# Kernel optimization log

Hardware: AMD Instinct MI355X
Metric: run time of the kernel (lower is better)

## Reference

```python
import jax, jax.numpy as jnp
import numpy as np

N_NODES = 50000
N_EDGES = 600000
LATENT = 128
IN_FEAT = 7
STEPS = 3
MLP_LAYERS = 2


def setup_inputs() -> dict:
    key = jax.random.key(0)
    ks = jax.random.split(key, 8)
    s = 0.05
    nodes = jax.random.normal(ks[0], (N_NODES, IN_FEAT), jnp.float32)
    senders = jax.random.randint(ks[1], (N_EDGES,), 0, N_NODES, jnp.int32)
    receivers = jax.random.randint(ks[2], (N_EDGES,), 0, N_NODES, jnp.int32)
    W_embed = jax.random.normal(ks[3], (IN_FEAT, LATENT), jnp.float32) * s
    b_embed = jnp.zeros((LATENT,), jnp.float32)
    mlp_W = jax.random.normal(ks[4], (STEPS, MLP_LAYERS, LATENT, LATENT), jnp.float32) * s
    mlp_b = jnp.zeros((STEPS, MLP_LAYERS, LATENT), jnp.float32)
    ln_scale = jnp.ones((STEPS, LATENT), jnp.float32)
    ln_bias = jnp.zeros((STEPS, LATENT), jnp.float32)
    W_dec = jax.random.normal(ks[5], (LATENT, IN_FEAT), jnp.float32) * s
    b_dec = jnp.zeros((IN_FEAT,), jnp.float32)
    return dict(nodes=nodes, senders=senders, receivers=receivers,
                W_embed=W_embed, b_embed=b_embed, mlp_W=mlp_W, mlp_b=mlp_b,
                ln_scale=ln_scale, ln_bias=ln_bias, W_dec=W_dec, b_dec=b_dec)


def _layer_norm(x, scale, bias, eps=1e-6):
    mu = jnp.mean(x, axis=-1, keepdims=True)
    var = jnp.var(x, axis=-1, keepdims=True)
    return (x - mu) * jax.lax.rsqrt(var + eps) * scale + bias


def reference(nodes, senders, receivers, W_embed, b_embed, mlp_W, mlp_b,
              ln_scale, ln_bias, W_dec, b_dec):
    n = nodes.shape[0]
    # symmetric normalization factors (jraph GraphConvolution default)
    ones = jnp.ones((senders.shape[0],), dtype=nodes.dtype)
    sender_deg = jax.ops.segment_sum(ones, senders, num_segments=n)
    receiver_deg = jax.ops.segment_sum(ones, receivers, num_segments=n)
    inv_sqrt_s = jax.lax.rsqrt(jnp.maximum(sender_deg, 1.0))[:, None]
    inv_sqrt_r = jax.lax.rsqrt(jnp.maximum(receiver_deg, 1.0))[:, None]

    # node embedder
    h = nodes @ W_embed + b_embed  # [N, LATENT]
    for step in range(mlp_W.shape[0]):
        # per-node MLP update (update_node_fn applied before aggregation)
        x = h
        for l in range(mlp_W.shape[1]):
            x = jax.nn.relu(x @ mlp_W[step, l] + mlp_b[step, l])
        # normalized gather -> scatter-sum aggregation
        x = x * inv_sqrt_s
        x = jax.ops.segment_sum(x[senders], receivers, num_segments=n)
        x = x * inv_sqrt_r
        # skip connection + layer norm
        h = _layer_norm(h + x, ln_scale[step], ln_bias[step])
    # decoder back to input feature size
    return h @ W_dec + b_dec  # [N, IN_FEAT]
```

## Files before the change

### kernel.cpp

```cpp
#include <hip/hip_runtime.h>

#define NN 50000
#define NE 600000
#define LAT 128
#define IN_F 7
#define CSR_W 64
#define HSTR 136

typedef __attribute__((ext_vector_type(8))) short bfrag;
typedef __attribute__((ext_vector_type(4))) float ffrag;
typedef __attribute__((ext_vector_type(2))) float f32x2;

__device__ inline unsigned short f2bf(float f) {
    unsigned int u = __float_as_uint(f);
    return (unsigned short)((u + 0x7FFFu + ((u >> 16) & 1u)) >> 16);
}
__device__ inline float bf2f(unsigned int b) { return __uint_as_float(b << 16); }


__global__ void k_prep(const float* __restrict__ W, unsigned short* __restrict__ Wp,
                       unsigned int* __restrict__ cnt) {
    int t = blockIdx.x * 256 + threadIdx.x;
    if (t < NN) cnt[t] = 0;
    if (t < 6 * 8 * 4 * 64) {
        int lane = t & 63;
        int ks = (t >> 6) & 3;
        int nt = (t >> 8) & 7;
        int mat = t >> 11;
        int n = nt * 16 + (lane & 15);
        int k0 = ks * 32 + (lane >> 4) * 8;
        const float* src = W + (size_t)mat * LAT * LAT;
        unsigned long long lo = 0, hi = 0;
#pragma unroll
        for (int j = 0; j < 4; ++j)
            lo |= (unsigned long long)f2bf(src[(k0 + j) * LAT + n]) << (16 * j);
#pragma unroll
        for (int j = 0; j < 4; ++j)
            hi |= (unsigned long long)f2bf(src[(k0 + 4 + j) * LAT + n]) << (16 * j);
        unsigned long long* dst = (unsigned long long*)(Wp + (size_t)t * 8);
        dst[0] = lo; dst[1] = hi;
    }
}


__global__ __launch_bounds__(256) void k_fused1(
    const int* __restrict__ s, const int* __restrict__ r,
    unsigned int* __restrict__ cnt, unsigned short* __restrict__ slot,
    const float* __restrict__ nodes, const float* __restrict__ We,
    const float* __restrict__ be,
    const unsigned short* __restrict__ W0p, const unsigned short* __restrict__ W1p,
    const float* __restrict__ b0, const float* __restrict__ b1,
    unsigned char* __restrict__ x, int build_blocks)
{
    __shared__ unsigned short hs[64][HSTR];
    int tid = threadIdx.x;

    if ((int)blockIdx.x < build_blocks) {
        int i = blockIdx.x * 256 + tid;
        if (i < NE) {
            int ss = s[i], rr = r[i];
            atomicAdd(&cnt[ss], 1u);
            unsigned int p = atomicAdd(&cnt[rr], 0x10000u) >> 16;
            if (p < CSR_W) slot[(size_t)rr * CSR_W + p] = (unsigned short)ss;
        }
        return;
    }

    int brow = ((int)blockIdx.x - build_blocks) * 64;
    int rows = NN - brow; if (rows > 64) rows = 64;

#pragma unroll
    for (int it = 0; it < 8; ++it) {
        int fi = it * 256 + tid;
        int rr = fi >> 5, cc = (fi & 31) << 2;
        if (rr < rows) {
            const float* nr = nodes + (size_t)(brow + rr) * IN_F;
            float o0 = be[cc], o1 = be[cc + 1], o2 = be[cc + 2], o3 = be[cc + 3];
#pragma unroll
            for (int k = 0; k < IN_F; ++k) {
                float nv = nr[k];
                const float* wk = We + k * LAT + cc;
                o0 += nv * wk[0]; o1 += nv * wk[1];
                o2 += nv * wk[2]; o3 += nv * wk[3];
            }
            unsigned long long pk = (unsigned long long)f2bf(o0)
                | ((unsigned long long)f2bf(o1) << 16)
                | ((unsigned long long)f2bf(o2) << 32)
                | ((unsigned long long)f2bf(o3) << 48);
            *(unsigned long long*)&hs[rr][cc] = pk;
        }
    }
    __syncthreads();

    int w = tid >> 6, lane = tid & 63;
    int mrow = w * 16 + (lane & 15);
    int koff = (lane >> 4) * 8;
    int ccol = lane & 15;
    int crow = w * 16 + (lane >> 4) * 4;

    float bia0[8], bia1[8];
#pragma unroll
    for (int nt = 0; nt < 8; ++nt) { bia0[nt] = b0[nt * 16 + ccol]; bia1[nt] = b1[nt * 16 + ccol]; }

    ffrag acc[8];
#pragma unroll
    for (int nt = 0; nt < 8; ++nt) acc[nt] = (ffrag)0.0f;
#pragma unroll
    for (int ks = 0; ks < 4; ++ks) {
        bfrag af = *(const bfrag*)&hs[mrow][ks * 32 + koff];
#pragma unroll
        for (int nt = 0; nt < 8; ++nt) {
            bfrag bf = *(const bfrag*)&W0p[(size_t)(((nt * 4) + ks) * 64 + lane) * 8];
            acc[nt] = __builtin_amdgcn_mfma_f32_16x16x32_bf16(af, bf, acc[nt], 0, 0, 0);
        }
    }
#pragma unroll
    for (int nt = 0; nt < 8; ++nt)
#pragma unroll
        for (int reg = 0; reg < 4; ++reg)
            hs[crow + reg][nt * 16 + ccol] = f2bf(fmaxf(acc[nt][reg] + bia0[nt], 0.f));
    __syncthreads();

#pragma unroll
    for (int nt = 0; nt < 8; ++nt) acc[nt] = (ffrag)0.0f;
#pragma unroll
    for (int ks = 0; ks < 4; ++ks) {
        bfrag af = *(const bfrag*)&hs[mrow][ks * 32 + koff];
#pragma unroll
        for (int nt = 0; nt < 8; ++nt) {
            bfrag bf = *(const bfrag*)&W1p[(size_t)(((nt * 4) + ks) * 64 + lane) * 8];
            acc[nt] = __builtin_amdgcn_mfma_f32_16x16x32_bf16(af, bf, acc[nt], 0, 0, 0);
        }
    }
    __syncthreads();
#pragma unroll
    for (int nt = 0; nt < 8; ++nt)
#pragma unroll
        for (int reg = 0; reg < 4; ++reg)
            hs[crow + reg][nt * 16 + ccol] = f2bf(fmaxf(acc[nt][reg] + bia1[nt], 0.f));
    __syncthreads();

#pragma unroll
    for (int it = 0; it < 8; ++it) {
        int fi = it * 256 + tid;
        int rr = fi >> 5, uc = fi & 31;
        if (rr < rows) {
            unsigned long long pk8 = *(unsigned long long*)&hs[rr][uc * 4];
            float f0 = bf2f((unsigned int)(pk8 & 0xFFFFu));
            float f1 = bf2f((unsigned int)((pk8 >> 16) & 0xFFFFu));
            float f2 = bf2f((unsigned int)((pk8 >> 32) & 0xFFFFu));
            float f3 = bf2f((unsigned int)((pk8 >> 48) & 0xFFFFu));
            int o = __builtin_amdgcn_cvt_pk_fp8_f32(f0, f1, 0, false);
            o = __builtin_amdgcn_cvt_pk_fp8_f32(f2, f3, o, true);
            *(int*)&x[(size_t)(brow + rr) * LAT + uc * 4] = o;
        }
    }
}


__global__ __launch_bounds__(256) void k_mlp2(
    const unsigned short* __restrict__ h,
    const unsigned short* __restrict__ W0p, const unsigned short* __restrict__ W1p,
    const float* __restrict__ b0, const float* __restrict__ b1,
    const unsigned int* __restrict__ cnt,
    unsigned char* __restrict__ x, int M)
{
    __shared__ unsigned short hs[64][HSTR];
    int brow = blockIdx.x * 64;
    int tid = threadIdx.x;
    int rows = M - brow; if (rows > 64) rows = 64;

#pragma unroll
    for (int it = 0; it < 8; ++it) {
        int fi = it * 256 + tid;
        int rr = fi >> 5, cc = (fi & 31) << 2;
        if (rr < rows)
            *(unsigned long long*)&hs[rr][cc] =
                *(const unsigned long long*)&h[(size_t)(brow + rr) * LAT + cc];
    }
    __syncthreads();

    int w = tid >> 6, lane = tid & 63;
    int mrow = w * 16 + (lane & 15);
    int koff = (lane >> 4) * 8;
    int ccol = lane & 15;
    int crow = w * 16 + (lane >> 4) * 4;

    float bia0[8], bia1[8];
#pragma unroll
    for (int nt = 0; nt < 8; ++nt) { bia0[nt] = b0[nt * 16 + ccol]; bia1[nt] = b1[nt * 16 + ccol]; }
    float iv[4];
#pragma unroll
    for (int reg = 0; reg < 4; ++reg) {
        int rw = brow + crow + reg;
        unsigned int ds = cnt[rw < NN ? rw : NN - 1] & 0xFFFFu;
        iv[reg] = rsqrtf((float)(ds > 1 ? ds : 1));
    }

    ffrag acc[8];
#pragma unroll
    for (int nt = 0; nt < 8; ++nt) acc[nt] = (ffrag)0.0f;
#pragma unroll
    for (int ks = 0; ks < 4; ++ks) {
        bfrag af = *(const bfrag*)&hs[mrow][ks * 32 + koff];
#pragma unroll
        for (int nt = 0; nt < 8; ++nt) {
            bfrag bf = *(const bfrag*)&W0p[(size_t)(((nt * 4) + ks) * 64 + lane) * 8];
            acc[nt] = __builtin_amdgcn_mfma_f32_16x16x32_bf16(af, bf, acc[nt], 0, 0, 0);
        }
    }
#pragma unroll
    for (int nt = 0; nt < 8; ++nt)
#pragma unroll
        for (int reg = 0; reg < 4; ++reg)
            hs[crow + reg][nt * 16 + ccol] = f2bf(fmaxf(acc[nt][reg] + bia0[nt], 0.f));
    __syncthreads();

#pragma unroll
    for (int nt = 0; nt < 8; ++nt) acc[nt] = (ffrag)0.0f;
#pragma unroll
    for (int ks = 0; ks < 4; ++ks) {
        bfrag af = *(const bfrag*)&hs[mrow][ks * 32 + koff];
#pragma unroll
        for (int nt = 0; nt < 8; ++nt) {
            bfrag bf = *(const bfrag*)&W1p[(size_t)(((nt * 4) + ks) * 64 + lane) * 8];
            acc[nt] = __builtin_amdgcn_mfma_f32_16x16x32_bf16(af, bf, acc[nt], 0, 0, 0);
        }
    }
    __syncthreads();
#pragma unroll
    for (int nt = 0; nt < 8; ++nt)
#pragma unroll
        for (int reg = 0; reg < 4; ++reg)
            hs[crow + reg][nt * 16 + ccol] =
                f2bf(fmaxf(acc[nt][reg] + bia1[nt], 0.f) * iv[reg]);
    __syncthreads();

#pragma unroll
    for (int it = 0; it < 8; ++it) {
        int fi = it * 256 + tid;
        int rr = fi >> 5, uc = fi & 31;
        if (rr < rows) {
            unsigned long long pk8 = *(unsigned long long*)&hs[rr][uc * 4];
            float f0 = bf2f((unsigned int)(pk8 & 0xFFFFu));
            float f1 = bf2f((unsigned int)((pk8 >> 16) & 0xFFFFu));
            float f2 = bf2f((unsigned int)((pk8 >> 32) & 0xFFFFu));
            float f3 = bf2f((unsigned int)((pk8 >> 48) & 0xFFFFu));
            int o = __builtin_amdgcn_cvt_pk_fp8_f32(f0, f1, 0, false);
            o = __builtin_amdgcn_cvt_pk_fp8_f32(f2, f3, o, true);
            *(int*)&x[(size_t)(brow + rr) * LAT + uc * 4] = o;
        }
    }
}


__global__ __launch_bounds__(256) void k_agg(
    const unsigned char* __restrict__ x, unsigned short* __restrict__ h,
    const float* __restrict__ nodes, const float* __restrict__ We,
    const float* __restrict__ be,
    const unsigned int* __restrict__ cnt, const unsigned short* __restrict__ slot,
    const float* __restrict__ gamma, const float* __restrict__ beta,
    const float* __restrict__ Wd, const float* __restrict__ bd,
    float* __restrict__ outd, int mode)
{
    int lane = threadIdx.x & 63;
    int r = blockIdx.x * 4 + (threadIdx.x >> 6);
    if (r >= NN) return;

    int ct = (int)(cnt[r] >> 16);
    float ir = rsqrtf((float)(ct > 1 ? ct : 1));
    int c = ct > CSR_W ? CSR_W : ct;

    int myidx = (lane < c) ? (int)slot[(size_t)r * CSR_W + lane] : 0;

    int j0 = lane * 2;
    float ax0 = 0.f, ay0 = 0.f, ax1 = 0.f, ay1 = 0.f;
    float ax2 = 0.f, ay2 = 0.f, ax3 = 0.f, ay3 = 0.f;
    float ax4 = 0.f, ay4 = 0.f, ax5 = 0.f, ay5 = 0.f;
    float ax6 = 0.f, ay6 = 0.f, ax7 = 0.f, ay7 = 0.f;
    int e = 0;

    if (mode == 0) {
        float myinv = 0.f;
        if (lane < c) {
            unsigned int ds = cnt[myidx] & 0xFFFFu;
            myinv = rsqrtf((float)(ds > 1 ? ds : 1));
        }
        for (; e + 8 <= c; e += 8) {
            int s0 = __shfl(myidx, e),     s1 = __shfl(myidx, e + 1);
            int s2 = __shfl(myidx, e + 2), s3 = __shfl(myidx, e + 3);
            int s4 = __shfl(myidx, e + 4), s5 = __shfl(myidx, e + 5);
            int s6 = __shfl(myidx, e + 6), s7 = __shfl(myidx, e + 7);
            float w0 = __shfl(myinv, e),     w1 = __shfl(myinv, e + 1);
            float w2 = __shfl(myinv, e + 2), w3 = __shfl(myinv, e + 3);
            float w4 = __shfl(myinv, e + 4), w5 = __shfl(myinv, e + 5);
            float w6 = __shfl(myinv, e + 6), w7 = __shfl(myinv, e + 7);
            unsigned short v0 = *(const unsigned short*)&x[(size_t)s0 * LAT + j0];
            unsigned short v1 = *(const unsigned short*)&x[(size_t)s1 * LAT + j0];
            unsigned short v2 = *(const unsigned short*)&x[(size_t)s2 * LAT + j0];
            unsigned short v3 = *(const unsigned short*)&x[(size_t)s3 * LAT + j0];
            unsigned short v4 = *(const unsigned short*)&x[(size_t)s4 * LAT + j0];
            unsigned short v5 = *(const unsigned short*)&x[(size_t)s5 * LAT + j0];
            unsigned short v6 = *(const unsigned short*)&x[(size_t)s6 * LAT + j0];
            unsigned short v7 = *(const unsigned short*)&x[(size_t)s7 * LAT + j0];
            f32x2 d0 = __builtin_amdgcn_cvt_pk_f32_fp8((int)v0, false);
            f32x2 d1 = __builtin_amdgcn_cvt_pk_f32_fp8((int)v1, false);
            f32x2 d2 = __builtin_amdgcn_cvt_pk_f32_fp8((int)v2, false);
            f32x2 d3 = __builtin_amdgcn_cvt_pk_f32_fp8((int)v3, false);
            f32x2 d4 = __builtin_amdgcn_cvt_pk_f32_fp8((int)v4, false);
            f32x2 d5 = __builtin_amdgcn_cvt_pk_f32_fp8((int)v5, false);
            f32x2 d6 = __builtin_amdgcn_cvt_pk_f32_fp8((int)v6, false);
            f32x2 d7 = __builtin_amdgcn_cvt_pk_f32_fp8((int)v7, false);
            ax0 += d0.x * w0; ay0 += d0.y * w0;
            ax1 += d1.x * w1; ay1 += d1.y * w1;
            ax2 += d2.x * w2; ay2 += d2.y * w2;
            ax3 += d3.x * w3; ay3 += d3.y * w3;
            ax4 += d4.x * w4; ay4 += d4.y * w4;
            ax5 += d5.x * w5; ay5 += d5.y * w5;
            ax6 += d6.x * w6; ay6 += d6.y * w6;
            ax7 += d7.x * w7; ay7 += d7.y * w7;
        }
        for (; e < c; ++e) {
            int s0 = __shfl(myidx, e);
            float w0 = __shfl(myinv, e);
            unsigned short v0 = *(const unsigned short*)&x[(size_t)s0 * LAT + j0];
            f32x2 d0 = __builtin_amdgcn_cvt_pk_f32_fp8((int)v0, false);
            ax0 += d0.x * w0; ay0 += d0.y * w0;
        }
    } else {
        for (; e + 8 <= c; e += 8) {
            int s0 = __shfl(myidx, e),     s1 = __shfl(myidx, e + 1);
            int s2 = __shfl(myidx, e + 2), s3 = __shfl(myidx, e + 3);
            int s4 = __shfl(myidx, e + 4), s5 = __shfl(myidx, e + 5);
            int s6 = __shfl(myidx, e + 6), s7 = __shfl(myidx, e + 7);
            unsigned short v0 = *(const unsigned short*)&x[(size_t)s0 * LAT + j0];
            unsigned short v1 = *(const unsigned short*)&x[(size_t)s1 * LAT + j0];
            unsigned short v2 = *(const unsigned short*)&x[(size_t)s2 * LAT + j0];
            unsigned short v3 = *(const unsigned short*)&x[(size_t)s3 * LAT + j0];
            unsigned short v4 = *(const unsigned short*)&x[(size_t)s4 * LAT + j0];
            unsigned short v5 = *(const unsigned short*)&x[(size_t)s5 * LAT + j0];
            unsigned short v6 = *(const unsigned short*)&x[(size_t)s6 * LAT + j0];
            unsigned short v7 = *(const unsigned short*)&x[(size_t)s7 * LAT + j0];
            f32x2 d0 = __builtin_amdgcn_cvt_pk_f32_fp8((int)v0, false);
            f32x2 d1 = __builtin_amdgcn_cvt_pk_f32_fp8((int)v1, false);
            f32x2 d2 = __builtin_amdgcn_cvt_pk_f32_fp8((int)v2, false);
            f32x2 d3 = __builtin_amdgcn_cvt_pk_f32_fp8((int)v3, false);
            f32x2 d4 = __builtin_amdgcn_cvt_pk_f32_fp8((int)v4, false);
            f32x2 d5 = __builtin_amdgcn_cvt_pk_f32_fp8((int)v5, false);
            f32x2 d6 = __builtin_amdgcn_cvt_pk_f32_fp8((int)v6, false);
            f32x2 d7 = __builtin_amdgcn_cvt_pk_f32_fp8((int)v7, false);
            ax0 += d0.x; ay0 += d0.y;  ax1 += d1.x; ay1 += d1.y;
            ax2 += d2.x; ay2 += d2.y;  ax3 += d3.x; ay3 += d3.y;
            ax4 += d4.x; ay4 += d4.y;  ax5 += d5.x; ay5 += d5.y;
            ax6 += d6.x; ay6 += d6.y;  ax7 += d7.x; ay7 += d7.y;
        }
        for (; e < c; ++e) {
            int s0 = __shfl(myidx, e);
            unsigned short v0 = *(const unsigned short*)&x[(size_t)s0 * LAT + j0];
            f32x2 d0 = __builtin_amdgcn_cvt_pk_f32_fp8((int)v0, false);
            ax0 += d0.x; ay0 += d0.y;
        }
    }

    float a0 = (((ax0 + ax1) + (ax2 + ax3)) + ((ax4 + ax5) + (ax6 + ax7))) * ir;
    float a1 = (((ay0 + ay1) + (ay2 + ay3)) + ((ay4 + ay5) + (ay6 + ay7))) * ir;

    float v0, v1;
    if (mode == 0) {
        float o0 = be[j0], o1 = be[j0 + 1];
#pragma unroll
        for (int k = 0; k < IN_F; ++k) {
            float nv = nodes[(size_t)r * IN_F + k];
            o0 += nv * We[k * LAT + j0];
            o1 += nv * We[k * LAT + j0 + 1];
        }
        v0 = o0 + a0; v1 = o1 + a1;
    } else {
        unsigned int hv = *(const unsigned int*)&h[(size_t)r * LAT + j0];
        v0 = bf2f(hv & 0xFFFFu) + a0;
        v1 = bf2f(hv >> 16) + a1;
    }

    float sum = v0 + v1, sq = v0 * v0 + v1 * v1;
#pragma unroll
    for (int m = 1; m <= 32; m <<= 1) {
        sum += __shfl_xor(sum, m);
        sq  += __shfl_xor(sq, m);
    }
    float mu = sum * (1.f / LAT);
    float rs = rsqrtf(sq * (1.f / LAT) - mu * mu + 1e-6f);

    float o0 = (v0 - mu) * rs * gamma[j0] + beta[j0];
    float o1 = (v1 - mu) * rs * gamma[j0 + 1] + beta[j0 + 1];

    if (mode < 2) {
        *(unsigned int*)&h[(size_t)r * LAT + j0] =
            (unsigned int)f2bf(o0) | ((unsigned int)f2bf(o1) << 16);
    } else {
        const float* wd0 = Wd + j0 * IN_F;
        const float* wd1 = Wd + (j0 + 1) * IN_F;
#pragma unroll
        for (int f = 0; f < IN_F; ++f) {
            float pv = o0 * wd0[f] + o1 * wd1[f];
#pragma unroll
            for (int m = 1; m <= 32; m <<= 1) pv += __shfl_xor(pv, m);
            if (lane == 0) outd[(size_t)r * IN_F + f] = pv + bd[f];
        }
    }
}


extern "C" void kernel_launch(void* const* d_in, const int* in_sizes, int n_in,
                              void* d_out, int out_size, void* d_ws, size_t ws_size,
                              hipStream_t stream)
{
    const float* nodes   = (const float*)d_in[0];
    const int*   senders = (const int*)d_in[1];
    const int*   recvs   = (const int*)d_in[2];
    const float* W_embed = (const float*)d_in[3];
    const float* b_embed = (const float*)d_in[4];
    const float* mlp_W   = (const float*)d_in[5];
    const float* mlp_b   = (const float*)d_in[6];
    const float* ln_s    = (const float*)d_in[7];
    const float* ln_b    = (const float*)d_in[8];
    const float* W_dec   = (const float*)d_in[9];
    const float* b_dec   = (const float*)d_in[10];
    float* out = (float*)d_out;

    char* p = (char*)d_ws;
    auto alloc = [&](size_t bytes) -> char* {
        char* q = p; p += (bytes + 255) & ~(size_t)255; return q;
    };
    unsigned short* h    = (unsigned short*)alloc((size_t)NN * LAT * 2);
    unsigned char*  x    = (unsigned char*)alloc((size_t)NN * LAT);
    unsigned short* Wp   = (unsigned short*)alloc((size_t)6 * LAT * LAT * 2);
    unsigned int* cnt    = (unsigned int*)alloc((size_t)NN * 4);
    unsigned short* slot = (unsigned short*)alloc((size_t)NN * CSR_W * 2);

    k_prep<<<(NN + 255) / 256, 256, 0, stream>>>(mlp_W, Wp, cnt);

    int build_blocks = (NE + 255) / 256;
    int mlp_blocks   = (NN + 63) / 64;
    int agg_blocks   = (NN + 3) / 4;

    const float* b0 = mlp_b;
    k_fused1<<<build_blocks + mlp_blocks, 256, 0, stream>>>(
        senders, recvs, cnt, slot, nodes, W_embed, b_embed,
        Wp, Wp + (size_t)LAT * LAT, b0, b0 + LAT, x, build_blocks);

    k_agg<<<agg_blocks, 256, 0, stream>>>(
        x, h, nodes, W_embed, b_embed, cnt, slot,
        ln_s, ln_b, nullptr, nullptr, nullptr, 0);

    k_mlp2<<<mlp_blocks, 256, 0, stream>>>(
        h, Wp + (size_t)2 * LAT * LAT, Wp + (size_t)3 * LAT * LAT,
        b0 + 2 * LAT, b0 + 3 * LAT, cnt, x, NN);
    k_agg<<<agg_blocks, 256, 0, stream>>>(
        x, h, nodes, W_embed, b_embed, cnt, slot,
        ln_s + LAT, ln_b + LAT, nullptr, nullptr, nullptr, 1);

    k_mlp2<<<mlp_blocks, 256, 0, stream>>>(
        h, Wp + (size_t)4 * LAT * LAT, Wp + (size_t)5 * LAT * LAT,
        b0 + 4 * LAT, b0 + 5 * LAT, cnt, x, NN);
    k_agg<<<agg_blocks, 256, 0, stream>>>(
        x, h, nodes, W_embed, b_embed, cnt, slot,
        ln_s + 2 * LAT, ln_b + 2 * LAT, W_dec, b_dec, out, 2);
}
```

Before: 322.0 us.

## Split aggregation into column-half gather kernel plus separate layernorm finalize kernel

Each aggregation step is now split into two kernels. The first launches twice as many blocks, with each wave gathering one byte per lane for one 64-column half of a row, and writes fp32 partial sums to a new workspace buffer. The second kernel reads those sums, applies receiver normalization, the skip connection, layer norm and optional decode. The intent is more parallelism and more outstanding loads in the gather phase, at the cost of byte-sized loads, an extra fp32 round trip through memory of about 25.6 MB, and three extra launches.

Result: slower. 410.0 us (+27.3%).

```diff
diff --git a/kernel.cpp b/kernel.cpp
--- a/kernel.cpp
+++ b/kernel.cpp
@@ -16,6 +16,10 @@
     return (unsigned short)((u + 0x7FFFu + ((u >> 16) & 1u)) >> 16);
 }
 __device__ inline float bf2f(unsigned int b) { return __uint_as_float(b << 16); }
+__device__ inline float fp8tof(unsigned int b) {
+    f32x2 d = __builtin_amdgcn_cvt_pk_f32_fp8((int)b, false);
+    return d.x;
+}
 
 
 __global__ void k_prep(const float* __restrict__ W, unsigned short* __restrict__ Wp,
@@ -254,33 +258,26 @@
 }
 
 
-__global__ __launch_bounds__(256) void k_agg(
-    const unsigned char* __restrict__ x, unsigned short* __restrict__ h,
-    const float* __restrict__ nodes, const float* __restrict__ We,
-    const float* __restrict__ be,
+__global__ __launch_bounds__(256) void k_aggA(
+    const unsigned char* __restrict__ x,
     const unsigned int* __restrict__ cnt, const unsigned short* __restrict__ slot,
-    const float* __restrict__ gamma, const float* __restrict__ beta,
-    const float* __restrict__ Wd, const float* __restrict__ bd,
-    float* __restrict__ outd, int mode)
+    float* __restrict__ ps, int weighted)
 {
+    int half = blockIdx.x & 1;
+    int r = (blockIdx.x >> 1) * 4 + (threadIdx.x >> 6);
+    if (r >= NN) return;
     int lane = threadIdx.x & 63;
-    int r = blockIdx.x * 4 + (threadIdx.x >> 6);
-    if (r >= NN) return;
 
     int ct = (int)(cnt[r] >> 16);
-    float ir = rsqrtf((float)(ct > 1 ? ct : 1));
     int c = ct > CSR_W ? CSR_W : ct;
-
     int myidx = (lane < c) ? (int)slot[(size_t)r * CSR_W + lane] : 0;
 
-    int j0 = lane * 2;
-    float ax0 = 0.f, ay0 = 0.f, ax1 = 0.f, ay1 = 0.f;
-    float ax2 = 0.f, ay2 = 0.f, ax3 = 0.f, ay3 = 0.f;
-    float ax4 = 0.f, ay4 = 0.f, ax5 = 0.f, ay5 = 0.f;
-    float ax6 = 0.f, ay6 = 0.f, ax7 = 0.f, ay7 = 0.f;
+    const unsigned char* xb = x + half * 64 + lane;
+    float a0 = 0.f, a1 = 0.f, a2 = 0.f, a3 = 0.f;
+    float a4 = 0.f, a5 = 0.f, a6 = 0.f, a7 = 0.f;
     int e = 0;
 
-    if (mode == 0) {
+    if (weighted) {
         float myinv = 0.f;
         if (lane < c) {
             unsigned int ds = cnt[myidx] & 0xFFFFu;
@@ -295,37 +292,24 @@
             float w2 = __shfl(myinv, e + 2), w3 = __shfl(myinv, e + 3);
             float w4 = __shfl(myinv, e + 4), w5 = __shfl(myinv, e + 5);
             float w6 = __shfl(myinv, e + 6), w7 = __shfl(myinv, e + 7);
-            unsigned short v0 = *(const unsigned short*)&x[(size_t)s0 * LAT + j0];
-            unsigned short v1 = *(const unsigned short*)&x[(size_t)s1 * LAT + j0];
-            unsigned short v2 = *(const unsigned short*)&x[(size_t)s2 * LAT + j0];
-            unsigned short v3 = *(const unsigned short*)&x[(size_t)s3 * LAT + j0];
-            unsigned short v4 = *(const unsigned short*)&x[(size_t)s4 * LAT + j0];
-            unsigned short v5 = *(const unsigned short*)&x[(size_t)s5 * LAT + j0];
-            unsigned short v6 = *(const unsigned short*)&x[(size_t)s6 * LAT + j0];
-            unsigned short v7 = *(const unsigned short*)&x[(size_t)s7 * LAT + j0];
-            f32x2 d0 = __builtin_amdgcn_cvt_pk_f32_fp8((int)v0, false);
-            f32x2 d1 = __builtin_amdgcn_cvt_pk_f32_fp8((int)v1, false);
-            f32x2 d2 = __builtin_amdgcn_cvt_pk_f32_fp8((int)v2, false);
-            f32x2 d3 = __builtin_amdgcn_cvt_pk_f32_fp8((int)v3, false);
-            f32x2 d4 = __builtin_amdgcn_cvt_pk_f32_fp8((int)v4, false);
-            f32x2 d5 = __builtin_amdgcn_cvt_pk_f32_fp8((int)v5, false);
-            f32x2 d6 = __builtin_amdgcn_cvt_pk_f32_fp8((int)v6, false);
-            f32x2 d7 = __builtin_amdgcn_cvt_pk_f32_fp8((int)v7, false);
-            ax0 += d0.x * w0; ay0 += d0.y * w0;
-            ax1 += d1.x * w1; ay1 += d1.y * w1;
-            ax2 += d2.x * w2; ay2 += d2.y * w2;
-            ax3 += d3.x * w3; ay3 += d3.y * w3;
-            ax4 += d4.x * w4; ay4 += d4.y * w4;
-            ax5 += d5.x * w5; ay5 += d5.y * w5;
-            ax6 += d6.x * w6; ay6 += d6.y * w6;
-            ax7 += d7.x * w7; ay7 += d7.y * w7;
+            unsigned int b0 = xb[(size_t)s0 * LAT];
+            unsigned int b1 = xb[(size_t)s1 * LAT];
+            unsigned int b2 = xb[(size_t)s2 * LAT];
+            unsigned int b3 = xb[(size_t)s3 * LAT];
+            unsigned int b4 = xb[(size_t)s4 * LAT];
+            unsigned int b5 = xb[(size_t)s5 * LAT];
+            unsigned int b6 = xb[(size_t)s6 * LAT];
+            unsigned int b7 = xb[(size_t)s7 * LAT];
+            a0 += fp8tof(b0) * w0; a1 += fp8tof(b1) * w1;
+            a2 += fp8tof(b2) * w2; a3 += fp8tof(b3) * w3;
+            a4 += fp8tof(b4) * w4; a5 += fp8tof(b5) * w5;
+            a6 += fp8tof(b6) * w6; a7 += fp8tof(b7) * w7;
         }
         for (; e < c; ++e) {
             int s0 = __shfl(myidx, e);
             float w0 = __shfl(myinv, e);
-            unsigned short v0 = *(const unsigned short*)&x[(size_t)s0 * LAT + j0];
-            f32x2 d0 = __builtin_amdgcn_cvt_pk_f32_fp8((int)v0, false);
-            ax0 += d0.x * w0; ay0 += d0.y * w0;
+            unsigned int b0 = xb[(size_t)s0 * LAT];
+            a0 += fp8tof(b0) * w0;
         }
     } else {
         for (; e + 8 <= c; e += 8) {
@@ -333,37 +317,50 @@
             int s2 = __shfl(myidx, e + 2), s3 = __shfl(myidx, e + 3);
             int s4 = __shfl(myidx, e + 4), s5 = __shfl(myidx, e + 5);
             int s6 = __shfl(myidx, e + 6), s7 = __shfl(myidx, e + 7);
-            unsigned short v0 = *(const unsigned short*)&x[(size_t)s0 * LAT + j0];
-            unsigned short v1 = *(const unsigned short*)&x[(size_t)s1 * LAT + j0];
-            unsigned short v2 = *(const unsigned short*)&x[(size_t)s2 * LAT + j0];
-            unsigned short v3 = *(const unsigned short*)&x[(size_t)s3 * LAT + j0];
-            unsigned short v4 = *(const unsigned short*)&x[(size_t)s4 * LAT + j0];
-            unsigned short v5 = *(const unsigned short*)&x[(size_t)s5 * LAT + j0];
-            unsigned short v6 = *(const unsigned short*)&x[(size_t)s6 * LAT + j0];
-            unsigned short v7 = *(const unsigned short*)&x[(size_t)s7 * LAT + j0];
-            f32x2 d0 = __builtin_amdgcn_cvt_pk_f32_fp8((int)v0, false);
-            f32x2 d1 = __builtin_amdgcn_cvt_pk_f32_fp8((int)v1, false);
-            f32x2 d2 = __builtin_amdgcn_cvt_pk_f32_fp8((int)v2, false);
-            f32x2 d3 = __builtin_amdgcn_cvt_pk_f32_fp8((int)v3, false);
-            f32x2 d4 = __builtin_amdgcn_cvt_pk_f32_fp8((int)v4, false);
-            f32x2 d5 = __builtin_amdgcn_cvt_pk_f32_fp8((int)v5, false);
-            f32x2 d6 = __builtin_amdgcn_cvt_pk_f32_fp8((int)v6, false);
-            f32x2 d7 = __builtin_amdgcn_cvt_pk_f32_fp8((int)v7, false);
-            ax0 += d0.x; ay0 += d0.y;  ax1 += d1.x; ay1 += d1.y;
-            ax2 += d2.x; ay2 += d2.y;  ax3 += d3.x; ay3 += d3.y;
-            ax4 += d4.x; ay4 += d4.y;  ax5 += d5.x; ay5 += d5.y;
-            ax6 += d6.x; ay6 += d6.y;  ax7 += d7.x; ay7 += d7.y;
+            unsigned int b0 = xb[(size_t)s0 * LAT];
+            unsigned int b1 = xb[(size_t)s1 * LAT];
+            unsigned int b2 = xb[(size_t)s2 * LAT];
+            unsigned int b3 = xb[(size_t)s3 * LAT];
+            unsigned int b4 = xb[(size_t)s4 * LAT];
+            unsigned int b5 = xb[(size_t)s5 * LAT];
+            unsigned int b6 = xb[(size_t)s6 * LAT];
+            unsigned int b7 = xb[(size_t)s7 * LAT];
+            a0 += fp8tof(b0); a1 += fp8tof(b1);
+            a2 += fp8tof(b2); a3 += fp8tof(b3);
+            a4 += fp8tof(b4); a5 += fp8tof(b5);
+            a6 += fp8tof(b6); a7 += fp8tof(b7);
         }
         for (; e < c; ++e) {
             int s0 = __shfl(myidx, e);
-            unsigned short v0 = *(const unsigned short*)&x[(size_t)s0 * LAT + j0];
-            f32x2 d0 = __builtin_amdgcn_cvt_pk_f32_fp8((int)v0, false);
-            ax0 += d0.x; ay0 += d0.y;
-        }
-    }
-
-    float a0 = (((ax0 + ax1) + (ax2 + ax3)) + ((ax4 + ax5) + (ax6 + ax7))) * ir;
-    float a1 = (((ay0 + ay1) + (ay2 + ay3)) + ((ay4 + ay5) + (ay6 + ay7))) * ir;
+            unsigned int b0 = xb[(size_t)s0 * LAT];
+            a0 += fp8tof(b0);
+        }
+    }
+
+    float acc = ((a0 + a1) + (a2 + a3)) + ((a4 + a5) + (a6 + a7));
+    ps[(size_t)r * LAT + half * 64 + lane] = acc;
+}
+
+
+__global__ __launch_bounds__(256) void k_fin(
+    const float* __restrict__ ps, unsigned short* __restrict__ h,
+    const float* __restrict__ nodes, const float* __restrict__ We,
+    const float* __restrict__ be,
+    const unsigned int* __restrict__ cnt,
+    const float* __restrict__ gamma, const float* __restrict__ beta,
+    const float* __restrict__ Wd, const float* __restrict__ bd,
+    float* __restrict__ outd, int mode)
+{
+    int lane = threadIdx.x & 63;
+    int r = blockIdx.x * 4 + (threadIdx.x >> 6);
+    if (r >= NN) return;
+    int j0 = lane * 2;
+
+    int ct = (int)(cnt[r] >> 16);
+    float ir = rsqrtf((float)(ct > 1 ? ct : 1));
+
+    float2 av = *(const float2*)&ps[(size_t)r * LAT + j0];
+    float a0 = av.x * ir, a1 = av.y * ir;
 
     float v0, v1;
     if (mode == 0) {
@@ -433,6 +430,7 @@
     };
     unsigned short* h    = (unsigned short*)alloc((size_t)NN * LAT * 2);
     unsigned char*  x    = (unsigned char*)alloc((size_t)NN * LAT);
+    float*          ps   = (float*)alloc((size_t)NN * LAT * 4);
     unsigned short* Wp   = (unsigned short*)alloc((size_t)6 * LAT * LAT * 2);
     unsigned int* cnt    = (unsigned int*)alloc((size_t)NN * 4);
     unsigned short* slot = (unsigned short*)alloc((size_t)NN * CSR_W * 2);
@@ -441,28 +439,29 @@
 
     int build_blocks = (NE + 255) / 256;
     int mlp_blocks   = (NN + 63) / 64;
-    int agg_blocks   = (NN + 3) / 4;
+    int aggA_blocks  = 2 * ((NN + 3) / 4);
+    int fin_blocks   = (NN + 3) / 4;
 
     const float* b0 = mlp_b;
     k_fused1<<<build_blocks + mlp_blocks, 256, 0, stream>>>(
         senders, recvs, cnt, slot, nodes, W_embed, b_embed,
         Wp, Wp + (size_t)LAT * LAT, b0, b0 + LAT, x, build_blocks);
 
-    k_agg<<<agg_blocks, 256, 0, stream>>>(
-        x, h, nodes, W_embed, b_embed, cnt, slot,
-        ln_s, ln_b, nullptr, nullptr, nullptr, 0);
+    k_aggA<<<aggA_blocks, 256, 0, stream>>>(x, cnt, slot, ps, 1);
+    k_fin<<<fin_blocks, 256, 0, stream>>>(ps, h, nodes, W_embed, b_embed, cnt,
+                                          ln_s, ln_b, nullptr, nullptr, nullptr, 0);
 
     k_mlp2<<<mlp_blocks, 256, 0, stream>>>(
         h, Wp + (size_t)2 * LAT * LAT, Wp + (size_t)3 * LAT * LAT,
         b0 + 2 * LAT, b0 + 3 * LAT, cnt, x, NN);
-    k_agg<<<agg_blocks, 256, 0, stream>>>(
-        x, h, nodes, W_embed, b_embed, cnt, slot,
-        ln_s + LAT, ln_b + LAT, nullptr, nullptr, nullptr, 1);
+    k_aggA<<<aggA_blocks, 256, 0, stream>>>(x, cnt, slot, ps, 0);
+    k_fin<<<fin_blocks, 256, 0, stream>>>(ps, h, nodes, W_embed, b_embed, cnt,
+                                          ln_s + LAT, ln_b + LAT, nullptr, nullptr, nullptr, 1);
 
     k_mlp2<<<mlp_blocks, 256, 0, stream>>>(
         h, Wp + (size_t)4 * LAT * LAT, Wp + (size_t)5 * LAT * LAT,
         b0 + 4 * LAT, b0 + 5 * LAT, cnt, x, NN);
-    k_agg<<<agg_blocks, 256, 0, stream>>>(
-        x, h, nodes, W_embed, b_embed, cnt, slot,
-        ln_s + 2 * LAT, ln_b + 2 * LAT, W_dec, b_dec, out, 2);
-}
+    k_aggA<<<aggA_blocks, 256, 0, stream>>>(x, cnt, slot, ps, 0);
+    k_fin<<<fin_blocks, 256, 0, stream>>>(ps, h, nodes, W_embed, b_embed, cnt,
+                                          ln_s + 2 * LAT, ln_b + 2 * LAT, W_dec, b_dec, out, 2);
+}
```

## Build CSR counts in LDS per node range instead of global atomics

Applied to the files above, without the earlier changes.

The edge-bucketing phase now runs as 32 blocks. Each block owns a contiguous range of node ids, scans every sender/receiver pair with vectorized int4 loads, and counts degrees and assigns receiver slots with shared-memory atomics. It then writes its counts to global memory, which removes the separate zeroing of the count array in the prep kernel. The aim is to avoid contended global atomics. In exchange, every block rereads the full edge list, and the build now rests on only 32 blocks, which could lengthen the critical path before aggregation.

Result: slower. 632.8 us (+96.5%).

```diff
diff --git a/kernel.cpp b/kernel.cpp
--- a/kernel.cpp
+++ b/kernel.cpp
@@ -6,6 +6,8 @@
 #define IN_F 7
 #define CSR_W 64
 #define HSTR 136
+#define NRANGE 32
+#define RNGSZ ((NN + NRANGE - 1) / NRANGE)
 
 typedef __attribute__((ext_vector_type(8))) short bfrag;
 typedef __attribute__((ext_vector_type(4))) float ffrag;
@@ -18,28 +20,25 @@
 __device__ inline float bf2f(unsigned int b) { return __uint_as_float(b << 16); }
 
 
-__global__ void k_prep(const float* __restrict__ W, unsigned short* __restrict__ Wp,
-                       unsigned int* __restrict__ cnt) {
+__global__ void k_prep(const float* __restrict__ W, unsigned short* __restrict__ Wp) {
     int t = blockIdx.x * 256 + threadIdx.x;
-    if (t < NN) cnt[t] = 0;
-    if (t < 6 * 8 * 4 * 64) {
-        int lane = t & 63;
-        int ks = (t >> 6) & 3;
-        int nt = (t >> 8) & 7;
-        int mat = t >> 11;
-        int n = nt * 16 + (lane & 15);
-        int k0 = ks * 32 + (lane >> 4) * 8;
-        const float* src = W + (size_t)mat * LAT * LAT;
-        unsigned long long lo = 0, hi = 0;
-#pragma unroll
-        for (int j = 0; j < 4; ++j)
-            lo |= (unsigned long long)f2bf(src[(k0 + j) * LAT + n]) << (16 * j);
-#pragma unroll
-        for (int j = 0; j < 4; ++j)
-            hi |= (unsigned long long)f2bf(src[(k0 + 4 + j) * LAT + n]) << (16 * j);
-        unsigned long long* dst = (unsigned long long*)(Wp + (size_t)t * 8);
-        dst[0] = lo; dst[1] = hi;
-    }
+    if (t >= 6 * 8 * 4 * 64) return;
+    int lane = t & 63;
+    int ks = (t >> 6) & 3;
+    int nt = (t >> 8) & 7;
+    int mat = t >> 11;
+    int n = nt * 16 + (lane & 15);
+    int k0 = ks * 32 + (lane >> 4) * 8;
+    const float* src = W + (size_t)mat * LAT * LAT;
+    unsigned long long lo = 0, hi = 0;
+#pragma unroll
+    for (int j = 0; j < 4; ++j)
+        lo |= (unsigned long long)f2bf(src[(k0 + j) * LAT + n]) << (16 * j);
+#pragma unroll
+    for (int j = 0; j < 4; ++j)
+        hi |= (unsigned long long)f2bf(src[(k0 + 4 + j) * LAT + n]) << (16 * j);
+    unsigned long long* dst = (unsigned long long*)(Wp + (size_t)t * 8);
+    dst[0] = lo; dst[1] = hi;
 }
 
 
@@ -56,13 +55,31 @@
     int tid = threadIdx.x;
 
     if ((int)blockIdx.x < build_blocks) {
-        int i = blockIdx.x * 256 + tid;
-        if (i < NE) {
-            int ss = s[i], rr = r[i];
-            atomicAdd(&cnt[ss], 1u);
-            unsigned int p = atomicAdd(&cnt[rr], 0x10000u) >> 16;
-            if (p < CSR_W) slot[(size_t)rr * CSR_W + p] = (unsigned short)ss;
-        }
+        unsigned int* lcnt = (unsigned int*)hs;
+        int rlo = (int)blockIdx.x * RNGSZ;
+        int rhi = rlo + RNGSZ; if (rhi > NN) rhi = NN;
+        int n = rhi - rlo;
+        for (int i = tid; i < n; i += 256) lcnt[i] = 0;
+        __syncthreads();
+
+        const int4* s4 = (const int4*)s;
+        const int4* r4 = (const int4*)r;
+        for (int i = tid; i < NE / 4; i += 256) {
+            int4 sv = s4[i];
+            int4 rv = r4[i];
+#pragma unroll
+            for (int j = 0; j < 4; ++j) {
+                int ss = (&sv.x)[j], rr = (&rv.x)[j];
+                if (ss >= rlo && ss < rhi)
+                    atomicAdd(&lcnt[ss - rlo], 1u);
+                if (rr >= rlo && rr < rhi) {
+                    unsigned int p = atomicAdd(&lcnt[rr - rlo], 0x10000u) >> 16;
+                    if (p < CSR_W) slot[(size_t)rr * CSR_W + p] = (unsigned short)ss;
+                }
+            }
+        }
+        __syncthreads();
+        for (int i = tid; i < n; i += 256) cnt[rlo + i] = lcnt[i];
         return;
     }
 
@@ -437,9 +454,9 @@
     unsigned int* cnt    = (unsigned int*)alloc((size_t)NN * 4);
     unsigned short* slot = (unsigned short*)alloc((size_t)NN * CSR_W * 2);
 
-    k_prep<<<(NN + 255) / 256, 256, 0, stream>>>(mlp_W, Wp, cnt);
-
-    int build_blocks = (NE + 255) / 256;
+    k_prep<<<(6 * 8 * 4 * 64 + 255) / 256, 256, 0, stream>>>(mlp_W, Wp);
+
+    int build_blocks = NRANGE;
     int mlp_blocks   = (NN + 63) / 64;
     int agg_blocks   = (NN + 3) / 4;
 
```
